# Kernel tuning notes

Hardware: AMD Instinct MI355X
Metric: run time of the kernel (lower is better)

Reference implementation:

```python
import math
import jax, jax.numpy as jnp
import numpy as np

D_MODEL = 256
D2 = 2 * D_MODEL
NHEADS = 8
NLAYERS = 6
FFN = 1024
Q, B, S = 300, 16, 1024


def _ln(x, eps=1e-5):
    m = jnp.mean(x, axis=-1, keepdims=True)
    v = jnp.mean((x - m) ** 2, axis=-1, keepdims=True)
    return (x - m) / jnp.sqrt(v + eps)


def _mlp2(x, W1, b1, W2, b2):
    return jnp.maximum(x @ W1 + b1, 0.0) @ W2 + b2


def _sine_embed(pos, d_model):
    # pos: [Q, B, 2] -> [Q, B, d_model]
    fd = d_model // 2
    dim_t = jnp.arange(fd, dtype=jnp.float32)
    dim_t = 10000.0 ** (2.0 * jnp.floor(dim_t / 2.0) / fd)
    scale = 2.0 * math.pi
    px = (pos[:, :, 0] * scale)[:, :, None] / dim_t
    py = (pos[:, :, 1] * scale)[:, :, None] / dim_t

    def inter(p):
        q, b, _ = p.shape
        return jnp.stack((jnp.sin(p[:, :, 0::2]), jnp.cos(p[:, :, 1::2])), axis=3).reshape(q, b, -1)

    return jnp.concatenate((inter(py), inter(px)), axis=2)


def _pairwise_iou(b):
    # b: [B, Q, 4] xyxy -> [B, Q, Q]
    area = (b[..., 2] - b[..., 0]) * (b[..., 3] - b[..., 1])
    lt = jnp.maximum(b[:, :, None, :2], b[:, None, :, :2])
    rb = jnp.minimum(b[:, :, None, 2:], b[:, None, :, 2:])
    wh = jnp.clip(rb - lt, 0.0)
    inter = wh[..., 0] * wh[..., 1]
    union = area[:, :, None] + area[:, None, :] - inter
    return inter / union


def _mha(q, k, v, Wq, Wk, Wv, Wo, bias=None):
    # q: [L,B,D], k/v: [S,B,D]
    L, Bb, D = q.shape
    Ss = k.shape[0]
    hd = D // NHEADS
    qh = (q @ Wq).reshape(L, Bb, NHEADS, hd).transpose(1, 2, 0, 3)  # [B,H,L,hd]
    kh = (k @ Wk).reshape(Ss, Bb, NHEADS, hd).transpose(1, 2, 0, 3)
    vh = (v @ Wv).reshape(Ss, Bb, NHEADS, hd).transpose(1, 2, 0, 3)
    logits = jnp.einsum('bhqd,bhkd->bhqk', qh, kh) / jnp.sqrt(jnp.float32(hd))
    if bias is not None:
        logits = logits + bias[:, None]  # broadcast over heads
    a = jax.nn.softmax(logits, axis=-1)
    o = jnp.einsum('bhqk,bhkd->bhqd', a, vh).transpose(2, 0, 1, 3).reshape(L, Bb, D)
    return o @ Wo


def setup_inputs() -> dict:
    key = jax.random.key(0)
    ks = iter(jax.random.split(key, 40))
    f32 = jnp.float32
    d = D_MODEL
    sc = 0.02
    inp = {
        'tgt': jax.random.normal(next(ks), (Q, B, D2), f32),
        'memory': jax.random.normal(next(ks), (S, B, D2), f32),
        'pos': jax.random.normal(next(ks), (S, B, D2), f32),
        'query_pos': jax.random.normal(next(ks), (Q, B, d), f32),
        # query_scale MLP (d->d->d)
        'qs_W1': jax.random.normal(next(ks), (d, d), f32) * sc, 'qs_b1': jnp.zeros((d,), f32),
        'qs_W2': jax.random.normal(next(ks), (d, d), f32) * sc, 'qs_b2': jnp.zeros((d,), f32),
        # ref_point_head MLP (d->d->2)
        'rp_W1': jax.random.normal(next(ks), (d, d), f32) * sc, 'rp_b1': jnp.zeros((d,), f32),
        'rp_W2': jax.random.normal(next(ks), (d, 2), f32) * sc, 'rp_b2': jnp.zeros((2,), f32),
        # bbox_embed_func MLP (d->d->4)
        'bb_W1': jax.random.normal(next(ks), (d, d), f32) * sc, 'bb_b1': jnp.zeros((d,), f32),
        'bb_W2': jax.random.normal(next(ks), (d, 4), f32) * sc, 'bb_b2': jnp.zeros((4,), f32),
    }
    for name in ['sa_Wq', 'sa_Wk', 'sa_Wv', 'sa_Wo', 'ca_Wq', 'ca_Wk', 'ca_Wv', 'ca_Wo']:
        inp[name] = jax.random.normal(next(ks), (NLAYERS, D2, D2), f32) * sc
    inp['ff_W1'] = jax.random.normal(next(ks), (NLAYERS, D2, FFN), f32) * sc
    inp['ff_b1'] = jnp.zeros((NLAYERS, FFN), f32)
    inp['ff_W2'] = jax.random.normal(next(ks), (NLAYERS, FFN, D2), f32) * sc
    inp['ff_b2'] = jnp.zeros((NLAYERS, D2), f32)
    return inp


def reference(tgt, memory, pos, query_pos,
              qs_W1, qs_b1, qs_W2, qs_b2,
              rp_W1, rp_b1, rp_W2, rp_b2,
              bb_W1, bb_b1, bb_W2, bb_b2,
              sa_Wq, sa_Wk, sa_Wv, sa_Wo,
              ca_Wq, ca_Wk, ca_Wv, ca_Wo,
              ff_W1, ff_b1, ff_W2, ff_b2):
    d = D_MODEL
    output = tgt
    ref_before = _mlp2(query_pos, rp_W1, rp_b1, rp_W2, rp_b2)          # [Q,B,2]
    reference_points = jax.nn.sigmoid(ref_before).transpose(1, 0, 2)   # [B,Q,2]
    qp2 = jnp.concatenate((query_pos, query_pos), axis=-1)             # [Q,B,2d]
    for l in range(NLAYERS):
        obj_center = reference_points.transpose(1, 0, 2)               # [Q,B,2]
        pos_transform = _mlp2(output[..., d:], qs_W1, qs_b1, qs_W2, qs_b2)
        qs = _sine_embed(obj_center, d) * pos_transform                # [Q,B,d]
        tmp = _mlp2(output[..., d:], bb_W1, bb_b1, bb_W2, bb_b2)       # [Q,B,4]
        tmp = tmp.at[..., :2].add(ref_before)
        coord = jax.nn.sigmoid(tmp)                                    # cxcywh
        cx, cy, w, h = coord[..., 0], coord[..., 1], coord[..., 2], coord[..., 3]
        boxes = jnp.stack((cx - 0.5 * w, cy - 0.5 * h, cx + 0.5 * w, cy + 0.5 * h),
                          axis=-1).transpose(1, 0, 2)                  # [B,Q,4]
        gious = jax.lax.stop_gradient(_pairwise_iou(boxes))            # [B,Q,Q]
        cs = (cx + cy).transpose(1, 0)                                 # [B,Q]
        cxcys = jax.lax.stop_gradient((cs[:, :, None] > cs[:, None, :]).astype(output.dtype))
        bias = gious + cxcys                                            # [B,Q,Q]
        qs2 = jnp.concatenate((qs, qs), axis=-1)                        # [Q,B,2d]
        # self-attention with giou/cxcy bias
        qsa = output + qp2
        sa = _mha(qsa, qsa, output, sa_Wq[l], sa_Wk[l], sa_Wv[l], sa_Wo[l], bias=bias)
        output = _ln(output + sa)
        # cross-attention, sine-modulated query
        ca = _mha(output + qp2 + qs2, memory + pos, memory,
                  ca_Wq[l], ca_Wk[l], ca_Wv[l], ca_Wo[l])
        output = _ln(output + ca)
        ff = jnp.maximum(output @ ff_W1[l] + ff_b1[l], 0.0) @ ff_W2[l] + ff_b2[l]
        output = _ln(output + ff)
    return output[None]  # [1,Q,B,2d]
```

## Files before the change

kernel.cpp:

```cpp
#include <hip/hip_runtime.h>
#include <cmath>

#define QLEN 300
#define BATCH 16
#define SLEN 1024
#define DM 256
#define DD 512
#define FFND 1024
#define NQROWS (QLEN*BATCH)
#define NMROWS (SLEN*BATCH)
#define LQPAD 304
#define SAKPAD 320

typedef __attribute__((ext_vector_type(8))) short short8;
typedef __attribute__((ext_vector_type(4))) float f32x4;
typedef __attribute__((ext_vector_type(4))) unsigned short ushort4_;

__device__ __forceinline__ float sigmoidf_(float x){ return 1.f/(1.f+expf(-x)); }

__device__ __forceinline__ unsigned short f2bf(float x){
  unsigned u = __float_as_uint(x);
  unsigned r = (u + 0x7FFFu + ((u >> 16) & 1u)) >> 16;
  return (unsigned short)r;
}
__device__ __forceinline__ float bf2f(unsigned short u){
  return __uint_as_float(((unsigned)u) << 16);
}

__device__ __forceinline__ void gload16(const void* g, void* l) {
  __builtin_amdgcn_global_load_lds((const __attribute__((address_space(1))) unsigned int*)g,
                                   (__attribute__((address_space(3))) unsigned int*)l, 16, 0, 0);
}

__global__ __launch_bounds__(256) void transpose_cvt(
    const float* __restrict__ W, unsigned short* __restrict__ Wt, int K, int N,
    size_t zsrc, size_t zdst)
{
  __shared__ float T[32][33];
  int n0 = blockIdx.x*32, k0 = blockIdx.y*32;
  size_t zs = (size_t)blockIdx.z * zsrc;
  size_t zd = (size_t)blockIdx.z * zdst;
  int tx = threadIdx.x & 31, ty = threadIdx.x >> 5;
  #pragma unroll
  for (int j = 0; j < 32; j += 8)
    T[ty+j][tx] = W[zs + (size_t)(k0+ty+j)*N + n0+tx];
  __syncthreads();
  #pragma unroll
  for (int j = 0; j < 32; j += 8)
    Wt[zd + (size_t)(n0+ty+j)*K + k0+tx] = f2bf(T[tx][ty+j]);
}

__global__ void concat_bias(const float* __restrict__ b1, const float* __restrict__ b2,
                            float* __restrict__ out)
{
  int i = blockIdx.x*256 + threadIdx.x;
  if (i < 256) out[i] = b1[i];
  else if (i < 512) out[i] = b2[i-256];
}

template<int BM, int OUTMODE, bool RELU>
__global__ __launch_bounds__(256) void gemm2(
    const unsigned short* __restrict__ Ab, const unsigned short* __restrict__ Wt,
    const float* __restrict__ bias, void* __restrict__ Cptr,
    int M, int N, int K, int lda, int Laux)
{
  __shared__ __align__(16) unsigned short As[2][BM*64];
  __shared__ __align__(16) unsigned short Bs[2][128*64];
  const int tid = threadIdx.x;
  const int w = tid >> 6, lane = tid & 63;
  const int bm = blockIdx.y*BM, bn = blockIdx.x*128;
  const int wm = w >> 1, wn = w & 1;
  const int c = lane & 15, hi = lane >> 4;
  constexpr int MR = (BM + 31)/32 < 1 ? 1 : BM/32;
  f32x4 acc[MR < 1 ? 1 : MR][4] = {};
  const int lrow8 = lane >> 3;
  const int lcol  = ((lane & 7) ^ lrow8) << 3;
  const int nt = K >> 6;

  auto stage = [&](int buf, int k0) {
    #pragma unroll
    for (int it = 0; it < BM/32; ++it) {
      int r = it*32 + w*8;
      gload16(&Ab[(size_t)(bm + r + lrow8)*lda + k0 + lcol], &As[buf][r*64]);
    }
    #pragma unroll
    for (int it = 0; it < 4; ++it) {
      int r = it*32 + w*8;
      gload16(&Wt[(size_t)(bn + r + lrow8)*K + k0 + lcol], &Bs[buf][r*64]);
    }
  };

  stage(0, 0);
  for (int t = 0; t < nt; ++t) {
    const int cur = t & 1;
    if (t + 1 < nt) {
      stage(cur ^ 1, (t+1) << 6);
      if constexpr (BM == 32)      asm volatile("s_waitcnt vmcnt(5)" ::: "memory");
      else if constexpr (BM == 64) asm volatile("s_waitcnt vmcnt(6)" ::: "memory");
      else                         asm volatile("s_waitcnt vmcnt(8)" ::: "memory");
    } else {
      asm volatile("s_waitcnt vmcnt(0)" ::: "memory");
    }
// ... 79 lines not shown
      gload16(&Wt[(size_t)(bn + r + lrow8)*K + k0 + lcol], &Bs[buf][r*64]);
    }
  };

  stage(0, 0);
  for (int t = 0; t < nt; ++t) {
    const int cur = t & 1;
    if (t + 1 < nt) {
      stage(cur ^ 1, (t+1) << 6);
      if constexpr (BM == 64) asm volatile("s_waitcnt vmcnt(6)" ::: "memory");
      else                    asm volatile("s_waitcnt vmcnt(8)" ::: "memory");
    } else {
      asm volatile("s_waitcnt vmcnt(0)" ::: "memory");
    }
    __builtin_amdgcn_s_barrier();
    #pragma unroll
    for (int ks = 0; ks < 2; ++ks) {
      short8 a[MR], bf[4];
      #pragma unroll
      for (int mr = 0; mr < MR; ++mr) {
        int m = wm*(BM/2) + mr*16 + c;
        a[mr] = *reinterpret_cast<const short8*>(&As[cur][m*64 + ((ks*32 + hi*8) ^ ((m&7)<<3))]);
      }
      #pragma unroll
      for (int nr = 0; nr < 4; ++nr) {
        int n = wn*64 + nr*16 + c;
        bf[nr] = *reinterpret_cast<const short8*>(&Bs[cur][n*64 + ((ks*32 + hi*8) ^ ((n&7)<<3))]);
      }
      #pragma unroll
      for (int mr = 0; mr < MR; ++mr)
        #pragma unroll
        for (int nr = 0; nr < 4; ++nr)
          acc[mr][nr] = __builtin_amdgcn_mfma_f32_16x16x32_bf16(a[mr], bf[nr], acc[mr][nr], 0, 0, 0);
    }
    asm volatile("s_waitcnt lgkmcnt(0)" ::: "memory");
    __builtin_amdgcn_sched_barrier(0);
    __builtin_amdgcn_s_barrier();
  }
  #pragma unroll
  for (int mr = 0; mr < MR; ++mr) {
    #pragma unroll
    for (int nr = 0; nr < 4; ++nr) {
      int colg = bn + wn*64 + nr*16 + c;
      int h = colg >> 6, dl = colg & 63;
      int q0 = qt + wm*(BM/2) + mr*16 + hi*4;
      ushort4_ pack;
      #pragma unroll
      for (int r = 0; r < 4; ++r) pack[r] = f2bf(acc[mr][nr][r]);
      *reinterpret_cast<ushort4_*>(&VT[((size_t)(b*8 + h)*64 + dl)*Lkpad + q0]) = pack;
    }
  }
}

template<int AMODE, bool OUTBF16, bool RELU>
__global__ __launch_bounds__(256) void gemm_mfma(
    const void* __restrict__ Aptr, const float* __restrict__ A2,
    const unsigned short* __restrict__ Wt, const float* __restrict__ bias,
    void* __restrict__ Cptr, int M, int N, int K, int lda)
{
  __shared__ __align__(16) unsigned short As[64][72];
  __shared__ __align__(16) unsigned short Bs[64][72];
  const int tid = threadIdx.x;
  const int bm = blockIdx.y*64, bn = blockIdx.x*64;
  const int w = tid >> 6, lane = tid & 63;
  const int wm = w >> 1, wn = w & 1;
  const int c = lane & 15, hi = lane >> 4;
  const int sr = tid >> 3, sk = (tid & 7) * 8;
  f32x4 acc[2][2] = {};
  for (int k0 = 0; k0 < K; k0 += 64) {
    #pragma unroll
    for (int it = 0; it < 2; ++it) {
      int m = sr + it*32;
      if (AMODE == 0) {
        const unsigned short* Ab = (const unsigned short*)Aptr;
        short8 v = *reinterpret_cast<const short8*>(&Ab[(size_t)(bm+m)*lda + k0 + sk]);
        *reinterpret_cast<short8*>(&As[m][sk]) = v;
      } else {
        const float* Af = (const float*)Aptr;
        size_t base = (size_t)(bm+m)*lda + k0 + sk;
        float4 f0 = *reinterpret_cast<const float4*>(&Af[base]);
        float4 f1 = *reinterpret_cast<const float4*>(&Af[base+4]);
        short8 v;
        v[0]=(short)f2bf(f0.x); v[1]=(short)f2bf(f0.y); v[2]=(short)f2bf(f0.z); v[3]=(short)f2bf(f0.w);
        v[4]=(short)f2bf(f1.x); v[5]=(short)f2bf(f1.y); v[6]=(short)f2bf(f1.z); v[7]=(short)f2bf(f1.w);
        *reinterpret_cast<short8*>(&As[m][sk]) = v;
      }
      short8 bv = *reinterpret_cast<const short8*>(&Wt[(size_t)(bn+m)*K + k0 + sk]);
      *reinterpret_cast<short8*>(&Bs[m][sk]) = bv;
    }
    __syncthreads();
    #pragma unroll
    for (int ks = 0; ks < 2; ++ks) {
      short8 a0 = *reinterpret_cast<const short8*>(&As[wm*32 + c][ks*32 + hi*8]);
      short8 a1 = *reinterpret_cast<const short8*>(&As[wm*32 + 16 + c][ks*32 + hi*8]);
      short8 b0 = *reinterpret_cast<const short8*>(&Bs[wn*32 + c][ks*32 + hi*8]);
      short8 b1 = *reinterpret_cast<const short8*>(&Bs[wn*32 + 16 + c][ks*32 + hi*8]);
      acc[0][0] = __builtin_amdgcn_mfma_f32_16x16x32_bf16(a0, b0, acc[0][0], 0, 0, 0);
      acc[0][1] = __builtin_amdgcn_mfma_f32_16x16x32_bf16(a0, b1, acc[0][1], 0, 0, 0);
      acc[1][0] = __builtin_amdgcn_mfma_f32_16x16x32_bf16(a1, b0, acc[1][0], 0, 0, 0);
      acc[1][1] = __builtin_amdgcn_mfma_f32_16x16x32_bf16(a1, b1, acc[1][1], 0, 0, 0);
    }
    __syncthreads();
  }
  #pragma unroll
  for (int mf = 0; mf < 2; ++mf) {
    #pragma unroll
    for (int nf = 0; nf < 2; ++nf) {
      int colg = bn + wn*32 + nf*16 + c;
      float bv = bias ? bias[colg] : 0.f;
      #pragma unroll
      for (int r = 0; r < 4; ++r) {
        int rowg = bm + wm*32 + mf*16 + hi*4 + r;
        float v = acc[mf][nf][r] + bv;
        if (RELU) v = fmaxf(v, 0.f);
        if (OUTBF16) ((unsigned short*)Cptr)[(size_t)rowg*N + colg] = f2bf(v);
        else         ((float*)Cptr)[(size_t)rowg*N + colg] = v;
      }
    }
  }
}

__global__ __launch_bounds__(256) void gemm_mfma_split(
    const unsigned short* __restrict__ Ab, const unsigned short* __restrict__ Wt,
    const float* __restrict__ bias, unsigned short* __restrict__ C1, float* __restrict__ C2,
    int M, int N, int K, int lda)
{
  __shared__ __align__(16) unsigned short As[64][72];
  __shared__ __align__(16) unsigned short Bs[64][72];
  const int tid = threadIdx.x;
  const int bm = blockIdx.y*64, bn = blockIdx.x*64;
  const int w = tid >> 6, lane = tid & 63;
  const int wm = w >> 1, wn = w & 1;
  const int c = lane & 15, hi = lane >> 4;
  const int sr = tid >> 3, sk = (tid & 7) * 8;
  f32x4 acc[2][2] = {};
  for (int k0 = 0; k0 < K; k0 += 64) {
    #pragma unroll
    for (int it = 0; it < 2; ++it) {
      int m = sr + it*32;
      short8 v = *reinterpret_cast<const short8*>(&Ab[(size_t)(bm+m)*lda + k0 + sk]);
      *reinterpret_cast<short8*>(&As[m][sk]) = v;
      short8 bv = *reinterpret_cast<const short8*>(&Wt[(size_t)(bn+m)*K + k0 + sk]);
      *reinterpret_cast<short8*>(&Bs[m][sk]) = bv;
    }
    __syncthreads();
    #pragma unroll
    for (int ks = 0; ks < 2; ++ks) {
      short8 a0 = *reinterpret_cast<const short8*>(&As[wm*32 + c][ks*32 + hi*8]);
      short8 a1 = *reinterpret_cast<const short8*>(&As[wm*32 + 16 + c][ks*32 + hi*8]);
      short8 b0 = *reinterpret_cast<const short8*>(&Bs[wn*32 + c][ks*32 + hi*8]);
      short8 b1 = *reinterpret_cast<const short8*>(&Bs[wn*32 + 16 + c][ks*32 + hi*8]);
      acc[0][0] = __builtin_amdgcn_mfma_f32_16x16x32_bf16(a0, b0, acc[0][0], 0, 0, 0);
      acc[0][1] = __builtin_amdgcn_mfma_f32_16x16x32_bf16(a0, b1, acc[0][1], 0, 0, 0);
      acc[1][0] = __builtin_amdgcn_mfma_f32_16x16x32_bf16(a1, b0, acc[1][0], 0, 0, 0);
      acc[1][1] = __builtin_amdgcn_mfma_f32_16x16x32_bf16(a1, b1, acc[1][1], 0, 0, 0);
    }
    __syncthreads();
  }
  #pragma unroll
  for (int mf = 0; mf < 2; ++mf) {
    #pragma unroll
    for (int nf = 0; nf < 2; ++nf) {
      int colg = bn + wn*32 + nf*16 + c;
      float bv = bias[colg];
      #pragma unroll
      for (int r = 0; r < 4; ++r) {
        int rowg = bm + wm*32 + mf*16 + hi*4 + r;
        float v = fmaxf(acc[mf][nf][r] + bv, 0.f);
        if (colg < 256) C1[(size_t)rowg*256 + colg] = f2bf(v);
        else            C2[(size_t)rowg*256 + (colg-256)] = v;
      }
    }
  }
}
// ... 30 lines not shown

  float m_ = -1e30f, l_ = 0.f;
  f32x4 accO[4] = {};
  const int qbase = qt + w*16 + hi*4;

  auto stageKV = [&](int buf, int kt) {
    #pragma unroll
    for (int it = 0; it < 2; ++it) {
      int r = it*32 + w*8;
      int kr = kt + r + lrow8; if (MASK && kr > Lk-1) kr = Lk-1;
      gload16(&Kh[(kbase + kr)*64 + lcol], &Ks[buf][r*64]);
    }
    #pragma unroll
    for (int it = 0; it < 2; ++it) {
      int r = it*32 + w*8;
      gload16(&VT[((size_t)bh*64 + r + lrow8)*Lkpad + kt + lcol], &Vs[buf][r*64]);
    }
  };

  stageKV(0, t0 << 6);
  for (int t = t0; t < t1; ++t) {
    const int cur = (t - t0) & 1;
    const int kt = t << 6;
    float4 bs4[4];
    if (HAS_BIAS) {
      #pragma unroll
      for (int g = 0; g < 4; ++g)
        bs4[g] = *reinterpret_cast<const float4*>(
            &bias[((size_t)b*Lq + qrow)*Lk + kt + g*16 + hi*4]);
    }
    if (t + 1 < t1) {
      stageKV(cur ^ 1, (t+1) << 6);
      asm volatile("s_waitcnt vmcnt(4)" ::: "memory");
    } else {
      asm volatile("s_waitcnt vmcnt(0)" ::: "memory");
    }
    __builtin_amdgcn_s_barrier();
    f32x4 s[4] = {};
    __builtin_amdgcn_s_setprio(1);
    #pragma unroll
    for (int g = 0; g < 4; ++g) {
      int m = g*16 + c;
      short8 kb0 = *reinterpret_cast<const short8*>(&Ks[cur][m*64 + ((hi*8)      ^ ((m&7)<<3))]);
      short8 kb1 = *reinterpret_cast<const short8*>(&Ks[cur][m*64 + ((32 + hi*8) ^ ((m&7)<<3))]);
      s[g] = __builtin_amdgcn_mfma_f32_16x16x32_bf16(kb0, qf0, s[g], 0, 0, 0);
      s[g] = __builtin_amdgcn_mfma_f32_16x16x32_bf16(kb1, qf1, s[g], 0, 0, 0);
    }
    __builtin_amdgcn_s_setprio(0);
    float tmax = -1e30f;
    #pragma unroll
    for (int g = 0; g < 4; ++g) {
      #pragma unroll
      for (int r = 0; r < 4; ++r) {
        float v = s[g][r] * 0.125f;
        if (HAS_BIAS) v += ((const float*)&bs4[g])[r];
        if (MASK && (kt + g*16 + hi*4 + r >= Lk)) v = -1e30f;
        s[g][r] = v;
        tmax = fmaxf(tmax, v);
      }
    }
    tmax = fmaxf(tmax, __shfl_xor(tmax, 16));
    tmax = fmaxf(tmax, __shfl_xor(tmax, 32));
    float newm = fmaxf(m_, tmax);
    float corr = __expf(m_ - newm);
    m_ = newm;
    float psum = 0.f;
    #pragma unroll
    for (int g = 0; g < 4; ++g) {
      ushort4_ pp;
      #pragma unroll
      for (int r = 0; r < 4; ++r) {
        float e = __expf(s[g][r] - newm);
        psum += e;
        pp[r] = f2bf(e);
      }
      *reinterpret_cast<ushort4_*>(&Pl[w][c][g*16 + hi*4]) = pp;
    }
    psum += __shfl_xor(psum, 16);
    psum += __shfl_xor(psum, 32);
    l_ = l_*corr + psum;
    float corr4[4];
    #pragma unroll
    for (int r = 0; r < 4; ++r) corr4[r] = __shfl(corr, hi*4 + r);
    #pragma unroll
    for (int dg = 0; dg < 4; ++dg)
      #pragma unroll
      for (int r = 0; r < 4; ++r) accO[dg][r] *= corr4[r];
    __builtin_amdgcn_s_setprio(1);
    #pragma unroll
    for (int ks = 0; ks < 2; ++ks) {
      short8 pa = *reinterpret_cast<const short8*>(&Pl[w][c][ks*32 + hi*8]);
      #pragma unroll
      for (int dg = 0; dg < 4; ++dg) {
        int n = dg*16 + c;
        short8 vb = *reinterpret_cast<const short8*>(&Vs[cur][n*64 + ((ks*32 + hi*8) ^ ((n&7)<<3))]);
        accO[dg] = __builtin_amdgcn_mfma_f32_16x16x32_bf16(pa, vb, accO[dg], 0, 0, 0);
      }
    }
    __builtin_amdgcn_s_setprio(0);
    asm volatile("s_waitcnt lgkmcnt(0)" ::: "memory");
    __builtin_amdgcn_sched_barrier(0);
    __builtin_amdgcn_s_barrier();
  }
  if (NS == 1) {
    float l4[4];
    #pragma unroll
    for (int r = 0; r < 4; ++r) l4[r] = __shfl(l_, hi*4 + r);
    #pragma unroll
    for (int r = 0; r < 4; ++r) {
      int qg = qbase + r;
      if (qg < Lq) {
        float inv = 1.f / l4[r];
        #pragma unroll
        for (int dg = 0; dg < 4; ++dg)
          Ob[((size_t)qg*BATCH + b)*DD + h*64 + 16*dg + c] = f2bf(accO[dg][r] * inv);
      }
    }
  } else {
    int qc = qt + w*16 + c;
    if (hi == 0 && qc < Lq) {
      size_t rowml = ((size_t)sp*128 + bh)*LQPAD + qc;
      MLpart[rowml*2]     = m_;
      MLpart[rowml*2 + 1] = l_;
    }
    #pragma unroll
    for (int r = 0; r < 4; ++r) {
      int qg = qbase + r;
      if (qg < Lq) {
        size_t rowo = ((size_t)sp*128 + bh)*LQPAD + qg;
        #pragma unroll
        for (int dg = 0; dg < 4; ++dg)
          Opart[rowo*64 + dg*16 + c] = f2bf(accO[dg][r]);
      }
    }
  }
}

__global__ __launch_bounds__(256) void attn_reduce(
    const unsigned short* __restrict__ Opart, const float* __restrict__ MLpart,
    unsigned short* __restrict__ Ob, int Lq)
// ... 89 lines not shown
}

__global__ void sine_embed_kernel(const float* __restrict__ refb, float* __restrict__ sine)
{
  int idx = blockIdx.x*blockDim.x + threadIdx.x;
  if (idx >= NQROWS*DM) return;
  int r = idx >> 8, c = idx & 255;
  int j = c & 127;
  float coord = refb[r*2 + (c < 128 ? 1 : 0)];
  float s = sigmoidf_(coord);
  float freq = expf(-(float)(j >> 1) * (9.210340371976184f / 64.f));
  float v = s * 6.283185307179586f * freq;
  sine[idx] = (j & 1) ? cosf(v) : sinf(v);
}

__global__ void boxes_kernel(const float* __restrict__ t4, const float* __restrict__ refb,
                             float* __restrict__ boxes, float* __restrict__ cs)
{
  int idx = blockIdx.x*blockDim.x + threadIdx.x;
  if (idx >= NQROWS) return;
  int q = idx / BATCH, b = idx % BATCH;
  float cx = sigmoidf_(t4[idx*4+0] + refb[idx*2+0]);
  float cy = sigmoidf_(t4[idx*4+1] + refb[idx*2+1]);
  float w  = sigmoidf_(t4[idx*4+2]);
  float h  = sigmoidf_(t4[idx*4+3]);
  int o = b*QLEN + q;
  boxes[o*4+0] = cx - 0.5f*w;
  boxes[o*4+1] = cy - 0.5f*h;
  boxes[o*4+2] = cx + 0.5f*w;
  boxes[o*4+3] = cy + 0.5f*h;
  cs[o] = cx + cy;
}

__global__ void bias_kernel(const float* __restrict__ boxes, const float* __restrict__ cs,
                            float* __restrict__ bias)
{
  int idx = blockIdx.x*blockDim.x + threadIdx.x;
  const int QQ = QLEN*QLEN;
  if (idx >= BATCH*QQ) return;
  int b = idx / QQ, rem = idx - b*QQ;
  int i = rem / QLEN, j = rem - i*QLEN;
  float4 bi = *reinterpret_cast<const float4*>(&boxes[((size_t)b*QLEN + i)*4]);
  float4 bj = *reinterpret_cast<const float4*>(&boxes[((size_t)b*QLEN + j)*4]);
  float ai = (bi.z-bi.x)*(bi.w-bi.y);
  float aj = (bj.z-bj.x)*(bj.w-bj.y);
  float ltx = fmaxf(bi.x, bj.x), lty = fmaxf(bi.y, bj.y);
  float rbx = fminf(bi.z, bj.z), rby = fminf(bi.w, bj.w);
  float w = fmaxf(rbx-ltx, 0.f), h = fmaxf(rby-lty, 0.f);
  float inter = w*h;
  float iou = inter / (ai + aj - inter);
  bias[idx] = iou + ((cs[b*QLEN+i] > cs[b*QLEN+j]) ? 1.f : 0.f);
}

__global__ void add_qp2(const float* __restrict__ X, const float* __restrict__ qp,
                        unsigned short* __restrict__ out)
{
  int idx = blockIdx.x*blockDim.x + threadIdx.x;
  if (idx >= NQROWS*DD) return;
  int r = idx >> 9, c = idx & 511;
  out[idx] = f2bf(X[idx] + qp[(r<<8) + (c & 255)]);
}

__global__ void caq_kernel(const float* __restrict__ X, const float* __restrict__ qp,
                           const float* __restrict__ sine, const float* __restrict__ pt,
                           unsigned short* __restrict__ out)
{
  int idx = blockIdx.x*blockDim.x + threadIdx.x;
  if (idx >= NQROWS*DD) return;
  int r = idx >> 9, c = idx & 511;
  int c2 = (r<<8) + (c & 255);
  out[idx] = f2bf(X[idx] + qp[c2] + sine[c2]*pt[c2]);
}

__global__ void cvt_mem(const float* __restrict__ mem, const float* __restrict__ pos,
                        unsigned short* __restrict__ mb, unsigned short* __restrict__ mvb)
{
  int i = blockIdx.x*blockDim.x + threadIdx.x;
  if (i >= NMROWS*DD/8) return;
  size_t base = (size_t)i*8;
  float4 a0 = *reinterpret_cast<const float4*>(mem+base);
  float4 a1 = *reinterpret_cast<const float4*>(mem+base+4);
  float4 p0 = *reinterpret_cast<const float4*>(pos+base);
  float4 p1 = *reinterpret_cast<const float4*>(pos+base+4);
  short8 s1, s2;
  s1[0]=(short)f2bf(a0.x+p0.x); s1[1]=(short)f2bf(a0.y+p0.y); s1[2]=(short)f2bf(a0.z+p0.z); s1[3]=(short)f2bf(a0.w+p0.w);
  s1[4]=(short)f2bf(a1.x+p1.x); s1[5]=(short)f2bf(a1.y+p1.y); s1[6]=(short)f2bf(a1.z+p1.z); s1[7]=(short)f2bf(a1.w+p1.w);
  s2[0]=(short)f2bf(a0.x); s2[1]=(short)f2bf(a0.y); s2[2]=(short)f2bf(a0.z); s2[3]=(short)f2bf(a0.w);
  s2[4]=(short)f2bf(a1.x); s2[5]=(short)f2bf(a1.y); s2[6]=(short)f2bf(a1.z); s2[7]=(short)f2bf(a1.w);
  *reinterpret_cast<short8*>(mb+base)  = s1;
  *reinterpret_cast<short8*>(mvb+base) = s2;
}

__global__ __launch_bounds__(256) void ln_residual(float* __restrict__ X, const float* __restrict__ Y,
                                                   unsigned short* __restrict__ Xb)
{
  int row = blockIdx.x, tid = threadIdx.x;
  size_t base = (size_t)row*DD;
  float v0 = X[base+tid]     + Y[base+tid];
  float v1 = X[base+tid+256] + Y[base+tid+256];
  float s = v0+v1, sq = v0*v0+v1*v1;
  for (int off = 32; off; off >>= 1) { s += __shfl_down(s,off); sq += __shfl_down(sq,off); }
  __shared__ float ss[4], ssq[4];
  int wid = tid>>6, lane = tid&63;
  if (lane==0){ ss[wid]=s; ssq[wid]=sq; }
  __syncthreads();
  if (tid==0){
    float a=ss[0]+ss[1]+ss[2]+ss[3], bsum=ssq[0]+ssq[1]+ssq[2]+ssq[3];
    float mean = a*(1.f/DD);
    float var  = bsum*(1.f/DD) - mean*mean;
    ss[0]=mean; ssq[0]=rsqrtf(fmaxf(var,0.f)+1e-5f);
  }
  __syncthreads();
  float mean = ss[0], inv = ssq[0];
  float o0 = (v0-mean)*inv, o1 = (v1-mean)*inv;
  X[base+tid]     = o0;  Xb[base+tid]     = f2bf(o0);
  X[base+tid+256] = o1;  Xb[base+tid+256] = f2bf(o1);
}

__global__ void init_x(const float* __restrict__ t, float* __restrict__ X,
                       unsigned short* __restrict__ Xb, int n)
{
  int idx = blockIdx.x*blockDim.x + threadIdx.x;
  if (idx < n){ float v = t[idx]; X[idx]=v; Xb[idx]=f2bf(v); }
}

__global__ void copy_f32(const float* __restrict__ src, float* __restrict__ dst, int n)
{
  int idx = blockIdx.x*blockDim.x + threadIdx.x;
  if (idx < n) dst[idx] = src[idx];
}

extern "C" void kernel_launch(void* const* d_in, const int* in_sizes, int n_in,
                              void* d_out, int out_size, void* d_ws, size_t ws_size,
                              hipStream_t stream)
{
  const float* tgt       = (const float*)d_in[0];
  const float* memory    = (const float*)d_in[1];
  const float* pos       = (const float*)d_in[2];
  const float* query_pos = (const float*)d_in[3];
  const float* qs_W1 = (const float*)d_in[4];  const float* qs_b1 = (const float*)d_in[5];
  const float* qs_W2 = (const float*)d_in[6];  const float* qs_b2 = (const float*)d_in[7];
  const float* rp_W1 = (const float*)d_in[8];  const float* rp_b1 = (const float*)d_in[9];
  const float* rp_W2 = (const float*)d_in[10]; const float* rp_b2 = (const float*)d_in[11];
  const float* bb_W1 = (const float*)d_in[12]; const float* bb_b1 = (const float*)d_in[13];
  const float* bb_W2 = (const float*)d_in[14]; const float* bb_b2 = (const float*)d_in[15];
  const float* sa_Wq = (const float*)d_in[16]; const float* sa_Wk = (const float*)d_in[17];
  const float* sa_Wv = (const float*)d_in[18]; const float* sa_Wo = (const float*)d_in[19];
  const float* ca_Wq = (const float*)d_in[20]; const float* ca_Wk = (const float*)d_in[21];
  const float* ca_Wv = (const float*)d_in[22]; const float* ca_Wo = (const float*)d_in[23];
  const float* ff_W1 = (const float*)d_in[24]; const float* ff_b1 = (const float*)d_in[25];
  const float* ff_W2 = (const float*)d_in[26]; const float* ff_b2 = (const float*)d_in[27];

  float* F = (float*)d_ws;
  size_t o = 0;
  float* X    = F + o; o += (size_t)NQROWS*DD;
  float* RES  = F + o; o += (size_t)NQROWS*DD;
  float* SINE = F + o; o += (size_t)NQROWS*DM;
  float* PT   = F + o; o += (size_t)NQROWS*DM;
  float* BIAS = F + o; o += (size_t)BATCH*QLEN*QLEN;
  float* REFB = F + o; o += (size_t)NQROWS*2;
  float* T4   = F + o; o += (size_t)NQROWS*4;
  float* BOX  = F + o; o += (size_t)NQROWS*4;
  float* CS   = F + o; o += (size_t)NQROWS;
  float* ML   = F + o; o += (size_t)2*128*LQPAD*2;
  float* QBB  = F + o; o += 512;
  float* T256 = RES;
  unsigned short* U = (unsigned short*)(F + o);
  size_t u = 0;
  unsigned short* Xb   = U + u; u += (size_t)NQROWS*DD;
  unsigned short* QIN  = U + u; u += (size_t)NQROWS*DD;
  unsigned short* PQb  = U + u; u += (size_t)NQROWS*DD;
  unsigned short* PKb  = U + u; u += (size_t)NMROWS*DD;
  unsigned short* PVb  = U + u; u += (size_t)NMROWS*DD;
  unsigned short* VTsa = U + u; u += (size_t)128*64*SAKPAD;
  unsigned short* OPARTU = U + u; u += (size_t)2*128*LQPAD*64;
  unsigned short* T256b= U + u; u += (size_t)NQROWS*DM;
  unsigned short* MEMb = U + u; u += (size_t)NMROWS*DD;
  unsigned short* MEMVb= U + u; u += (size_t)NMROWS*DD;
  unsigned short* WtSqk= U + u; u += (size_t)6*2*DD*DD;
  unsigned short* WtSv = U + u; u += (size_t)6*DD*DD;
  unsigned short* WtSo = U + u; u += (size_t)6*DD*DD;
  unsigned short* WtCq = U + u; u += (size_t)6*DD*DD;
  unsigned short* WtCk = U + u; u += (size_t)6*DD*DD;
  unsigned short* WtCv = U + u; u += (size_t)6*DD*DD;
  unsigned short* WtCo = U + u; u += (size_t)6*DD*DD;
  unsigned short* WtF1 = U + u; u += (size_t)6*DD*FFND;
  unsigned short* WtF2 = U + u; u += (size_t)6*DD*FFND;
  unsigned short* WtQB = U + u; u += (size_t)2*DM*DM;
  unsigned short* WtQ2 = U + u; u += (size_t)DM*DM;
  unsigned short* QKb  = PQb;
  unsigned short* AOb  = QIN;
  unsigned short* HIDb = PKb;
  if (ws_size < o*sizeof(float) + u*sizeof(unsigned short)) return;

  dim3 B256(256);
  const int nTotal = NQROWS*DD;
  const size_t ZD = (size_t)DD*DD;

  transpose_cvt<<<dim3(16,16,6), B256, 0, stream>>>(sa_Wq, WtSqk,      DD, DD, ZD, 2*ZD);
  transpose_cvt<<<dim3(16,16,6), B256, 0, stream>>>(sa_Wk, WtSqk + ZD, DD, DD, ZD, 2*ZD);
  transpose_cvt<<<dim3(16,16,6), B256, 0, stream>>>(sa_Wv, WtSv, DD, DD, ZD, ZD);
  transpose_cvt<<<dim3(16,16,6), B256, 0, stream>>>(sa_Wo, WtSo, DD, DD, ZD, ZD);
  transpose_cvt<<<dim3(16,16,6), B256, 0, stream>>>(ca_Wq, WtCq, DD, DD, ZD, ZD);
  transpose_cvt<<<dim3(16,16,6), B256, 0, stream>>>(ca_Wk, WtCk, DD, DD, ZD, ZD);
  transpose_cvt<<<dim3(16,16,6), B256, 0, stream>>>(ca_Wv, WtCv, DD, DD, ZD, ZD);
  transpose_cvt<<<dim3(16,16,6), B256, 0, stream>>>(ca_Wo, WtCo, DD, DD, ZD, ZD);
  transpose_cvt<<<dim3(32,16,6), B256, 0, stream>>>(ff_W1, WtF1, DD, FFND, (size_t)DD*FFND, (size_t)DD*FFND);
  transpose_cvt<<<dim3(16,32,6), B256, 0, stream>>>(ff_W2, WtF2, FFND, DD, (size_t)DD*FFND, (size_t)DD*FFND);
  transpose_cvt<<<dim3(8,8,1),  B256, 0, stream>>>(qs_W1, WtQB,             DM, DM, (size_t)DM*DM, (size_t)DM*DM);
  transpose_cvt<<<dim3(8,8,1),  B256, 0, stream>>>(bb_W1, WtQB + (size_t)DM*DM, DM, DM, (size_t)DM*DM, (size_t)DM*DM);
  transpose_cvt<<<dim3(8,8,1),  B256, 0, stream>>>(qs_W2, WtQ2, DM, DM, (size_t)DM*DM, (size_t)DM*DM);
  concat_bias<<<dim3(2), B256, 0, stream>>>(qs_b1, bb_b1, QBB);

  init_x<<<dim3((nTotal+255)/256), B256, 0, stream>>>(tgt, X, Xb, nTotal);
  cvt_mem<<<dim3(NMROWS*DD/8/256), B256, 0, stream>>>(memory, pos, MEMb, MEMVb);
  gemm_f32<<<dim3(DM/64, NQROWS/64), B256, 0, stream>>>(query_pos, nullptr, rp_W1, rp_b1, T256, NQROWS, DM, DM, DM, 1);
  gemm_skinny<<<dim3(NQROWS/4), B256, 0, stream>>>(T256, rp_W2, rp_b2, REFB, NQROWS, 2, DM, DM);
  sine_embed_kernel<<<dim3((NQROWS*DM+255)/256), B256, 0, stream>>>(REFB, SINE);

  const int nredu = (128*QLEN + 3) / 4;
  const int qtiles = (QLEN + 63) / 64;
  for (int l = 0; l < 6; ++l) {
    const size_t wo = (size_t)l*DD*DD, fo = (size_t)l*DD*FFND;
    const float* fb1 = ff_b1 + (size_t)l*FFND;
    const float* fb2 = ff_b2 + (size_t)l*DD;

    gemm_mfma_split<<<dim3(8, NQROWS/64), B256, 0, stream>>>(Xb+DM, WtQB, QBB, T256b, T256, NQROWS, 512, DM, DD);
    gemm_mfma<0,false,false><<<dim3(DM/64, NQROWS/64), B256, 0, stream>>>(T256b, nullptr, WtQ2, qs_b2, PT, NQROWS, DM, DM, DM);
    gemm_skinny<<<dim3(NQROWS/4), B256, 0, stream>>>(T256, bb_W2, bb_b2, T4, NQROWS, 4, DM, DM);
    boxes_kernel<<<dim3((NQROWS+255)/256), B256, 0, stream>>>(T4, REFB, BOX, CS);
    bias_kernel<<<dim3((BATCH*QLEN*QLEN+255)/256), B256, 0, stream>>>(BOX, CS, BIAS);

    add_qp2<<<dim3((nTotal+255)/256), B256, 0, stream>>>(X, query_pos, QIN);
    gemm2<64,2,false><<<dim3(1024/128, NQROWS/64), B256, 0, stream>>>(QIN, WtSqk + (size_t)l*2*ZD, nullptr, QKb, NQROWS, 1024, DD, DD, QLEN);
    gemm2_vt<64><<<dim3(DD/128, BATCH*5), B256, 0, stream>>>(Xb, WtSv+wo, VTsa, QLEN, DD, DD, SAKPAD, 5);
    attn2<true,true,2><<<dim3(128, qtiles, 2), B256, 0, stream>>>(QKb, QKb, VTsa, BIAS, nullptr, OPARTU, ML, QLEN, QLEN, SAKPAD, 16, 16, 8);
    attn_reduce<<<dim3(nredu), B256, 0, stream>>>(OPARTU, ML, AOb, QLEN);
    gemm2<32,0,false><<<dim3(DD/128, NQROWS/32), B256, 0, stream>>>(AOb, WtSo+wo, nullptr, RES, NQROWS, DD, DD, DD, 0);
    ln_residual<<<dim3(NQROWS), B256, 0, stream>>>(X, RES, Xb);

    caq_kernel<<<dim3((nTotal+255)/256), B256, 0, stream>>>(X, query_pos, SINE, PT, QIN);
    gemm2<32,2,false><<<dim3(DD/128, NQROWS/32), B256, 0, stream>>>(QIN, WtCq+wo, nullptr, PQb, NQROWS, DD, DD, DD, QLEN);
    gemm2<128,2,false><<<dim3(DD/128, NMROWS/128), B256, 0, stream>>>(MEMb,  WtCk+wo, nullptr, PKb, NMROWS, DD, DD, DD, SLEN);
    gemm2_vt<128><<<dim3(DD/128, BATCH*8), B256, 0, stream>>>(MEMVb, WtCv+wo, PVb, SLEN, DD, DD, SLEN, 8);
    attn2<false,false,2><<<dim3(128, qtiles, 2), B256, 0, stream>>>(PQb, PKb, PVb, nullptr, nullptr, OPARTU, ML, QLEN, SLEN, SLEN, 8, 8, 0);
    attn_reduce<<<dim3(nredu), B256, 0, stream>>>(OPARTU, ML, AOb, QLEN);
    gemm2<32,0,false><<<dim3(DD/128, NQROWS/32), B256, 0, stream>>>(AOb, WtCo+wo, nullptr, RES, NQROWS, DD, DD, DD, 0);
    ln_residual<<<dim3(NQROWS), B256, 0, stream>>>(X, RES, Xb);

    gemm2<64,1,true ><<<dim3(FFND/128, NQROWS/64), B256, 0, stream>>>(Xb, WtF1+fo, fb1, HIDb, NQROWS, FFND, DD, DD, 0);
    gemm2<32,0,false><<<dim3(DD/128, NQROWS/32), B256, 0, stream>>>(HIDb, WtF2+fo, fb2, RES, NQROWS, DD, FFND, FFND, 0);
    ln_residual<<<dim3(NQROWS), B256, 0, stream>>>(X, RES, Xb);
  }

  copy_f32<<<dim3((nTotal+255)/256), B256, 0, stream>>>(X, (float*)d_out, out_size);
}
```

Baseline: 1.657 ms.

## Fuse query prep into LN kernels, fold softmax scale into weights, lazy rescale

Removes the standalone add_qp2 and caq_kernel passes by having the layer-norm residual kernels (and init_x) also emit the bf16 query inputs. The 1/sqrt(hd) factor is folded into the Q projection weights during transpose-convert, and the attention kernel only rescales its running max and accumulators when some lane's max grows by more than 8. The small qs_W2 GEMM moves from the old gemm_mfma kernel to gemm2. Together these cut elementwise passes and per-tile softmax work; the lazy rescale relies on bounded exponent growth, and folding the scale into bf16 weights changes rounding slightly.

```diff
diff --git a/kernel.cpp b/kernel.cpp
--- a/kernel.cpp
+++ b/kernel.cpp
@@ -34,7 +34,7 @@
 
 __global__ __launch_bounds__(256) void transpose_cvt(
     const float* __restrict__ W, unsigned short* __restrict__ Wt, int K, int N,
-    size_t zsrc, size_t zdst)
+    size_t zsrc, size_t zdst, float scale)
 {
   __shared__ float T[32][33];
   int n0 = blockIdx.x*32, k0 = blockIdx.y*32;
@@ -47,7 +47,7 @@
   __syncthreads();
   #pragma unroll
   for (int j = 0; j < 32; j += 8)
-    Wt[zd + (size_t)(n0+ty+j)*K + k0+tx] = f2bf(T[tx][ty+j]);
+    Wt[zd + (size_t)(n0+ty+j)*K + k0+tx] = f2bf(T[tx][ty+j] * scale);
 }
 
 __global__ void concat_bias(const float* __restrict__ b1, const float* __restrict__ b2,
@@ -233,74 +233,6 @@
   }
 }
 
-template<int AMODE, bool OUTBF16, bool RELU>
-__global__ __launch_bounds__(256) void gemm_mfma(
-    const void* __restrict__ Aptr, const float* __restrict__ A2,
-    const unsigned short* __restrict__ Wt, const float* __restrict__ bias,
-    void* __restrict__ Cptr, int M, int N, int K, int lda)
-{
-  __shared__ __align__(16) unsigned short As[64][72];
-  __shared__ __align__(16) unsigned short Bs[64][72];
-  const int tid = threadIdx.x;
-  const int bm = blockIdx.y*64, bn = blockIdx.x*64;
-  const int w = tid >> 6, lane = tid & 63;
-  const int wm = w >> 1, wn = w & 1;
-  const int c = lane & 15, hi = lane >> 4;
-  const int sr = tid >> 3, sk = (tid & 7) * 8;
-  f32x4 acc[2][2] = {};
-  for (int k0 = 0; k0 < K; k0 += 64) {
-    #pragma unroll
-    for (int it = 0; it < 2; ++it) {
-      int m = sr + it*32;
-      if (AMODE == 0) {
-        const unsigned short* Ab = (const unsigned short*)Aptr;
-        short8 v = *reinterpret_cast<const short8*>(&Ab[(size_t)(bm+m)*lda + k0 + sk]);
-        *reinterpret_cast<short8*>(&As[m][sk]) = v;
-      } else {
-        const float* Af = (const float*)Aptr;
-        size_t base = (size_t)(bm+m)*lda + k0 + sk;
-        float4 f0 = *reinterpret_cast<const float4*>(&Af[base]);
-        float4 f1 = *reinterpret_cast<const float4*>(&Af[base+4]);
-        short8 v;
-        v[0]=(short)f2bf(f0.x); v[1]=(short)f2bf(f0.y); v[2]=(short)f2bf(f0.z); v[3]=(short)f2bf(f0.w);
-        v[4]=(short)f2bf(f1.x); v[5]=(short)f2bf(f1.y); v[6]=(short)f2bf(f1.z); v[7]=(short)f2bf(f1.w);
-        *reinterpret_cast<short8*>(&As[m][sk]) = v;
-      }
-      short8 bv = *reinterpret_cast<const short8*>(&Wt[(size_t)(bn+m)*K + k0 + sk]);
-      *reinterpret_cast<short8*>(&Bs[m][sk]) = bv;
-    }
-    __syncthreads();
-    #pragma unroll
-    for (int ks = 0; ks < 2; ++ks) {
-      short8 a0 = *reinterpret_cast<const short8*>(&As[wm*32 + c][ks*32 + hi*8]);
-      short8 a1 = *reinterpret_cast<const short8*>(&As[wm*32 + 16 + c][ks*32 + hi*8]);
-      short8 b0 = *reinterpret_cast<const short8*>(&Bs[wn*32 + c][ks*32 + hi*8]);
-      short8 b1 = *reinterpret_cast<const short8*>(&Bs[wn*32 + 16 + c][ks*32 + hi*8]);
-      acc[0][0] = __builtin_amdgcn_mfma_f32_16x16x32_bf16(a0, b0, acc[0][0], 0, 0, 0);
-      acc[0][1] = __builtin_amdgcn_mfma_f32_16x16x32_bf16(a0, b1, acc[0][1], 0, 0, 0);
-      acc[1][0] = __builtin_amdgcn_mfma_f32_16x16x32_bf16(a1, b0, acc[1][0], 0, 0, 0);
-      acc[1][1] = __builtin_amdgcn_mfma_f32_16x16x32_bf16(a1, b1, acc[1][1], 0, 0, 0);
-    }
-    __syncthreads();
-  }
-  #pragma unroll
-  for (int mf = 0; mf < 2; ++mf) {
-    #pragma unroll
-    for (int nf = 0; nf < 2; ++nf) {
-      int colg = bn + wn*32 + nf*16 + c;
-      float bv = bias ? bias[colg] : 0.f;
-      #pragma unroll
-      for (int r = 0; r < 4; ++r) {
-        int rowg = bm + wm*32 + mf*16 + hi*4 + r;
-        float v = acc[mf][nf][r] + bv;
-        if (RELU) v = fmaxf(v, 0.f);
-        if (OUTBF16) ((unsigned short*)Cptr)[(size_t)rowg*N + colg] = f2bf(v);
-        else         ((float*)Cptr)[(size_t)rowg*N + colg] = v;
-      }
-    }
-  }
-}
-
 __global__ __launch_bounds__(256) void gemm_mfma_split(
     const unsigned short* __restrict__ Ab, const unsigned short* __restrict__ Wt,
     const float* __restrict__ bias, unsigned short* __restrict__ C1, float* __restrict__ C2,
@@ -437,7 +369,7 @@
     for (int g = 0; g < 4; ++g) {
       #pragma unroll
       for (int r = 0; r < 4; ++r) {
-        float v = s[g][r] * 0.125f;
+        float v = s[g][r];
         if (HAS_BIAS) v += ((const float*)&bs4[g])[r];
         if (MASK && (kt + g*16 + hi*4 + r >= Lk)) v = -1e30f;
         s[g][r] = v;
@@ -446,16 +378,26 @@
     }
     tmax = fmaxf(tmax, __shfl_xor(tmax, 16));
     tmax = fmaxf(tmax, __shfl_xor(tmax, 32));
-    float newm = fmaxf(m_, tmax);
-    float corr = __expf(m_ - newm);
-    m_ = newm;
+    if (!__all(tmax - m_ <= 8.f)) {
+      float newm = fmaxf(m_, tmax);
+      float corr = __expf(m_ - newm);
+      m_ = newm;
+      l_ *= corr;
+      float corr4[4];
+      #pragma unroll
+      for (int r = 0; r < 4; ++r) corr4[r] = __shfl(corr, hi*4 + r);
+      #pragma unroll
+      for (int dg = 0; dg < 4; ++dg)
+        #pragma unroll
+        for (int r = 0; r < 4; ++r) accO[dg][r] *= corr4[r];
+    }
     float psum = 0.f;
     #pragma unroll
     for (int g = 0; g < 4; ++g) {
       ushort4_ pp;
       #pragma unroll
       for (int r = 0; r < 4; ++r) {
-        float e = __expf(s[g][r] - newm);
+        float e = __expf(s[g][r] - m_);
         psum += e;
         pp[r] = f2bf(e);
       }
@@ -463,14 +405,7 @@
     }
     psum += __shfl_xor(psum, 16);
     psum += __shfl_xor(psum, 32);
-    l_ = l_*corr + psum;
-    float corr4[4];
-    #pragma unroll
-    for (int r = 0; r < 4; ++r) corr4[r] = __shfl(corr, hi*4 + r);
-    #pragma unroll
-    for (int dg = 0; dg < 4; ++dg)
-      #pragma unroll
-      for (int r = 0; r < 4; ++r) accO[dg][r] *= corr4[r];
+    l_ += psum;
     __builtin_amdgcn_s_setprio(1);
     #pragma unroll
     for (int ks = 0; ks < 2; ++ks) {
@@ -666,26 +601,6 @@
   bias[idx] = iou + ((cs[b*QLEN+i] > cs[b*QLEN+j]) ? 1.f : 0.f);
 }
 
-__global__ void add_qp2(const float* __restrict__ X, const float* __restrict__ qp,
-                        unsigned short* __restrict__ out)
-{
-  int idx = blockIdx.x*blockDim.x + threadIdx.x;
-  if (idx >= NQROWS*DD) return;
-  int r = idx >> 9, c = idx & 511;
-  out[idx] = f2bf(X[idx] + qp[(r<<8) + (c & 255)]);
-}
-
-__global__ void caq_kernel(const float* __restrict__ X, const float* __restrict__ qp,
-                           const float* __restrict__ sine, const float* __restrict__ pt,
-                           unsigned short* __restrict__ out)
-{
-  int idx = blockIdx.x*blockDim.x + threadIdx.x;
-  if (idx >= NQROWS*DD) return;
-  int r = idx >> 9, c = idx & 511;
-  int c2 = (r<<8) + (c & 255);
-  out[idx] = f2bf(X[idx] + qp[c2] + sine[c2]*pt[c2]);
-}
-
 __global__ void cvt_mem(const float* __restrict__ mem, const float* __restrict__ pos,
                         unsigned short* __restrict__ mb, unsigned short* __restrict__ mvb)
 {
@@ -705,8 +620,11 @@
   *reinterpret_cast<short8*>(mvb+base) = s2;
 }
 
-__global__ __launch_bounds__(256) void ln_residual(float* __restrict__ X, const float* __restrict__ Y,
-                                                   unsigned short* __restrict__ Xb)
+template<int EMIT>
+__global__ __launch_bounds__(256) void ln_residual_t(
+    float* __restrict__ X, const float* __restrict__ Y, unsigned short* __restrict__ Xb,
+    const float* __restrict__ qp, const float* __restrict__ sine, const float* __restrict__ pt,
+    unsigned short* __restrict__ QIN)
 {
   int row = blockIdx.x, tid = threadIdx.x;
   size_t base = (size_t)row*DD;
@@ -729,13 +647,25 @@
   float o0 = (v0-mean)*inv, o1 = (v1-mean)*inv;
   X[base+tid]     = o0;  Xb[base+tid]     = f2bf(o0);
   X[base+tid+256] = o1;  Xb[base+tid+256] = f2bf(o1);
-}
-
-__global__ void init_x(const float* __restrict__ t, float* __restrict__ X,
-                       unsigned short* __restrict__ Xb, int n)
+  if (EMIT >= 1) {
+    size_t c2 = (size_t)row*256 + tid;
+    float add = qp[c2];
+    if (EMIT == 2) add += sine[c2]*pt[c2];
+    QIN[base+tid]     = f2bf(o0 + add);
+    QIN[base+tid+256] = f2bf(o1 + add);
+  }
+}
+
+__global__ void init_x(const float* __restrict__ t, const float* __restrict__ qp,
+                       float* __restrict__ X, unsigned short* __restrict__ Xb,
+                       unsigned short* __restrict__ QIN, int n)
 {
   int idx = blockIdx.x*blockDim.x + threadIdx.x;
-  if (idx < n){ float v = t[idx]; X[idx]=v; Xb[idx]=f2bf(v); }
+  if (idx < n){
+    float v = t[idx]; X[idx]=v; Xb[idx]=f2bf(v);
+    int r = idx >> 9, c = idx & 511;
+    QIN[idx] = f2bf(v + qp[(r<<8) + (c & 255)]);
+  }
 }
 
 __global__ void copy_f32(const float* __restrict__ src, float* __restrict__ dst, int n)
@@ -810,23 +740,24 @@
   dim3 B256(256);
   const int nTotal = NQROWS*DD;
   const size_t ZD = (size_t)DD*DD;
-
-  transpose_cvt<<<dim3(16,16,6), B256, 0, stream>>>(sa_Wq, WtSqk,      DD, DD, ZD, 2*ZD);
-  transpose_cvt<<<dim3(16,16,6), B256, 0, stream>>>(sa_Wk, WtSqk + ZD, DD, DD, ZD, 2*ZD);
-  transpose_cvt<<<dim3(16,16,6), B256, 0, stream>>>(sa_Wv, WtSv, DD, DD, ZD, ZD);
-  transpose_cvt<<<dim3(16,16,6), B256, 0, stream>>>(sa_Wo, WtSo, DD, DD, ZD, ZD);
-  transpose_cvt<<<dim3(16,16,6), B256, 0, stream>>>(ca_Wq, WtCq, DD, DD, ZD, ZD);
-  transpose_cvt<<<dim3(16,16,6), B256, 0, stream>>>(ca_Wk, WtCk, DD, DD, ZD, ZD);
-  transpose_cvt<<<dim3(16,16,6), B256, 0, stream>>>(ca_Wv, WtCv, DD, DD, ZD, ZD);
-  transpose_cvt<<<dim3(16,16,6), B256, 0, stream>>>(ca_Wo, WtCo, DD, DD, ZD, ZD);
-  transpose_cvt<<<dim3(32,16,6), B256, 0, stream>>>(ff_W1, WtF1, DD, FFND, (size_t)DD*FFND, (size_t)DD*FFND);
-  transpose_cvt<<<dim3(16,32,6), B256, 0, stream>>>(ff_W2, WtF2, FFND, DD, (size_t)DD*FFND, (size_t)DD*FFND);
-  transpose_cvt<<<dim3(8,8,1),  B256, 0, stream>>>(qs_W1, WtQB,             DM, DM, (size_t)DM*DM, (size_t)DM*DM);
-  transpose_cvt<<<dim3(8,8,1),  B256, 0, stream>>>(bb_W1, WtQB + (size_t)DM*DM, DM, DM, (size_t)DM*DM, (size_t)DM*DM);
-  transpose_cvt<<<dim3(8,8,1),  B256, 0, stream>>>(qs_W2, WtQ2, DM, DM, (size_t)DM*DM, (size_t)DM*DM);
+  const size_t ZM = (size_t)DM*DM;
+
+  transpose_cvt<<<dim3(16,16,6), B256, 0, stream>>>(sa_Wq, WtSqk,      DD, DD, ZD, 2*ZD, 0.125f);
+  transpose_cvt<<<dim3(16,16,6), B256, 0, stream>>>(sa_Wk, WtSqk + ZD, DD, DD, ZD, 2*ZD, 1.f);
+  transpose_cvt<<<dim3(16,16,6), B256, 0, stream>>>(sa_Wv, WtSv, DD, DD, ZD, ZD, 1.f);
+  transpose_cvt<<<dim3(16,16,6), B256, 0, stream>>>(sa_Wo, WtSo, DD, DD, ZD, ZD, 1.f);
+  transpose_cvt<<<dim3(16,16,6), B256, 0, stream>>>(ca_Wq, WtCq, DD, DD, ZD, ZD, 0.125f);
+  transpose_cvt<<<dim3(16,16,6), B256, 0, stream>>>(ca_Wk, WtCk, DD, DD, ZD, ZD, 1.f);
+  transpose_cvt<<<dim3(16,16,6), B256, 0, stream>>>(ca_Wv, WtCv, DD, DD, ZD, ZD, 1.f);
+  transpose_cvt<<<dim3(16,16,6), B256, 0, stream>>>(ca_Wo, WtCo, DD, DD, ZD, ZD, 1.f);
+  transpose_cvt<<<dim3(32,16,6), B256, 0, stream>>>(ff_W1, WtF1, DD, FFND, (size_t)DD*FFND, (size_t)DD*FFND, 1.f);
+  transpose_cvt<<<dim3(16,32,6), B256, 0, stream>>>(ff_W2, WtF2, FFND, DD, (size_t)DD*FFND, (size_t)DD*FFND, 1.f);
+  transpose_cvt<<<dim3(8,8,1),  B256, 0, stream>>>(qs_W1, WtQB,      DM, DM, ZM, ZM, 1.f);
+  transpose_cvt<<<dim3(8,8,1),  B256, 0, stream>>>(bb_W1, WtQB + ZM, DM, DM, ZM, ZM, 1.f);
+  transpose_cvt<<<dim3(8,8,1),  B256, 0, stream>>>(qs_W2, WtQ2, DM, DM, ZM, ZM, 1.f);
   concat_bias<<<dim3(2), B256, 0, stream>>>(qs_b1, bb_b1, QBB);
 
-  init_x<<<dim3((nTotal+255)/256), B256, 0, stream>>>(tgt, X, Xb, nTotal);
+  init_x<<<dim3((nTotal+255)/256), B256, 0, stream>>>(tgt, query_pos, X, Xb, QIN, nTotal);
   cvt_mem<<<dim3(NMROWS*DD/8/256), B256, 0, stream>>>(memory, pos, MEMb, MEMVb);
   gemm_f32<<<dim3(DM/64, NQROWS/64), B256, 0, stream>>>(query_pos, nullptr, rp_W1, rp_b1, T256, NQROWS, DM, DM, DM, 1);
   gemm_skinny<<<dim3(NQROWS/4), B256, 0, stream>>>(T256, rp_W2, rp_b2, REFB, NQROWS, 2, DM, DM);
@@ -840,31 +771,29 @@
     const float* fb2 = ff_b2 + (size_t)l*DD;
 
     gemm_mfma_split<<<dim3(8, NQROWS/64), B256, 0, stream>>>(Xb+DM, WtQB, QBB, T256b, T256, NQROWS, 512, DM, DD);
-    gemm_mfma<0,false,false><<<dim3(DM/64, NQROWS/64), B256, 0, stream>>>(T256b, nullptr, WtQ2, qs_b2, PT, NQROWS, DM, DM, DM);
+    gemm2<32,0,false><<<dim3(DM/128, NQROWS/32), B256, 0, stream>>>(T256b, WtQ2, qs_b2, PT, NQROWS, DM, DM, DM, 0);
     gemm_skinny<<<dim3(NQROWS/4), B256, 0, stream>>>(T256, bb_W2, bb_b2, T4, NQROWS, 4, DM, DM);
     boxes_kernel<<<dim3((NQROWS+255)/256), B256, 0, stream>>>(T4, REFB, BOX, CS);
     bias_kernel<<<dim3((BATCH*QLEN*QLEN+255)/256), B256, 0, stream>>>(BOX, CS, BIAS);
 
-    add_qp2<<<dim3((nTotal+255)/256), B256, 0, stream>>>(X, query_pos, QIN);
     gemm2<64,2,false><<<dim3(1024/128, NQROWS/64), B256, 0, stream>>>(QIN, WtSqk + (size_t)l*2*ZD, nullptr, QKb, NQROWS, 1024, DD, DD, QLEN);
     gemm2_vt<64><<<dim3(DD/128, BATCH*5), B256, 0, stream>>>(Xb, WtSv+wo, VTsa, QLEN, DD, DD, SAKPAD, 5);
     attn2<true,true,2><<<dim3(128, qtiles, 2), B256, 0, stream>>>(QKb, QKb, VTsa, BIAS, nullptr, OPARTU, ML, QLEN, QLEN, SAKPAD, 16, 16, 8);
     attn_reduce<<<dim3(nredu), B256, 0, stream>>>(OPARTU, ML, AOb, QLEN);
     gemm2<32,0,false><<<dim3(DD/128, NQROWS/32), B256, 0, stream>>>(AOb, WtSo+wo, nullptr, RES, NQROWS, DD, DD, DD, 0);
-    ln_residual<<<dim3(NQROWS), B256, 0, stream>>>(X, RES, Xb);
-
-    caq_kernel<<<dim3((nTotal+255)/256), B256, 0, stream>>>(X, query_pos, SINE, PT, QIN);
+    ln_residual_t<2><<<dim3(NQROWS), B256, 0, stream>>>(X, RES, Xb, query_pos, SINE, PT, QIN);
+
     gemm2<32,2,false><<<dim3(DD/128, NQROWS/32), B256, 0, stream>>>(QIN, WtCq+wo, nullptr, PQb, NQROWS, DD, DD, DD, QLEN);
     gemm2<128,2,false><<<dim3(DD/128, NMROWS/128), B256, 0, stream>>>(MEMb,  WtCk+wo, nullptr, PKb, NMROWS, DD, DD, DD, SLEN);
     gemm2_vt<128><<<dim3(DD/128, BATCH*8), B256, 0, stream>>>(MEMVb, WtCv+wo, PVb, SLEN, DD, DD, SLEN, 8);
     attn2<false,false,2><<<dim3(128, qtiles, 2), B256, 0, stream>>>(PQb, PKb, PVb, nullptr, nullptr, OPARTU, ML, QLEN, SLEN, SLEN, 8, 8, 0);
     attn_reduce<<<dim3(nredu), B256, 0, stream>>>(OPARTU, ML, AOb, QLEN);
     gemm2<32,0,false><<<dim3(DD/128, NQROWS/32), B256, 0, stream>>>(AOb, WtCo+wo, nullptr, RES, NQROWS, DD, DD, DD, 0);
-    ln_residual<<<dim3(NQROWS), B256, 0, stream>>>(X, RES, Xb);
+    ln_residual_t<0><<<dim3(NQROWS), B256, 0, stream>>>(X, RES, Xb, nullptr, nullptr, nullptr, nullptr);
 
     gemm2<64,1,true ><<<dim3(FFND/128, NQROWS/64), B256, 0, stream>>>(Xb, WtF1+fo, fb1, HIDb, NQROWS, FFND, DD, DD, 0);
     gemm2<32,0,false><<<dim3(DD/128, NQROWS/32), B256, 0, stream>>>(HIDb, WtF2+fo, fb2, RES, NQROWS, DD, FFND, FFND, 0);
-    ln_residual<<<dim3(NQROWS), B256, 0, stream>>>(X, RES, Xb);
+    ln_residual_t<1><<<dim3(NQROWS), B256, 0, stream>>>(X, RES, Xb, query_pos, nullptr, nullptr, QIN);
   }
 
   copy_f32<<<dim3((nTotal+255)/256), B256, 0, stream>>>(X, (float*)d_out, out_size);
```

New measurement: 1.585 ms. 4.4% less time.
